# Kernel optimization log

Measured on AMD Instinct MI355X. Metric: run time of the kernel, lower is better.

The kernel has to match this reference:

```python
import jax, jax.numpy as jnp
import numpy as np

B, NAG = 8192, 16          # scenes, agents per scene
CIN, CH = 64, 128          # gnn_in_channels, gnn_out_channels
R2 = 8.0 * 8.0             # comm_range squared
BOX = 20.0                 # positions sampled uniformly in [0, BOX]^2


def _lin(k, fi, fo):
    k1, k2 = jax.random.split(k)
    s = 1.0 / np.sqrt(fi)
    W = jax.random.uniform(k1, (fi, fo), jnp.float32, -s, s)
    b = jax.random.uniform(k2, (fo,), jnp.float32, -s, s)
    return W, b


def setup_inputs() -> dict:
    key = jax.random.key(0)
    ks = jax.random.split(key, 10)
    x = jax.random.normal(ks[0], (B * NAG, CIN), jnp.float32)          # VAE mu per agent
    pos = jax.random.uniform(ks[1], (B, NAG, 2), jnp.float32) * BOX    # sensor xy positions
    W_rel1, b_rel1 = _lin(ks[2], CIN, CH)
    W_root1, _ = _lin(ks[3], CIN, CH)
    W_rel2, b_rel2 = _lin(ks[4], CH, CH)
    W_root2, _ = _lin(ks[5], CH, CH)
    Wh1, bh1 = _lin(ks[6], 2 * CH, 64)
    Wh2, bh2 = _lin(ks[7], 64, 32)
    Wh3, bh3 = _lin(ks[8], 32, 16)
    return dict(x=x, pos=pos, W_rel1=W_rel1, b_rel1=b_rel1, W_root1=W_root1,
                W_rel2=W_rel2, b_rel2=b_rel2, W_root2=W_root2,
                Wh1=Wh1, bh1=bh1, Wh2=Wh2, bh2=bh2, Wh3=Wh3, bh3=bh3)


def _graph_conv(h, adj, W_rel, b_rel, W_root):
    # PyG GraphConv (aggr='add'): out_i = W_rel @ sum_{j in N(i)} h_j + b_rel + W_root @ h_i
    nb = adj.shape[0]
    hb = h.reshape(nb, NAG, h.shape[-1])                 # [B, n, C]
    agg = jnp.einsum('bij,bjc->bic', adj, hb)            # neighbor sum within each scene
    return agg.reshape(h.shape[0], -1) @ W_rel + b_rel + h @ W_root


def reference(x, pos, W_rel1, b_rel1, W_root1, W_rel2, b_rel2, W_root2,
              Wh1, bh1, Wh2, bh2, Wh3, bh3):
    # radius_graph (batch-isolated, loop=False) as a per-scene dense mask
    diff = pos[:, :, None, :] - pos[:, None, :, :]       # [B, n, n, 2]
    d2 = jnp.sum(diff * diff, axis=-1)                   # [B, n, n]
    eye = jnp.eye(NAG, dtype=bool)
    adj = ((d2 <= R2) & ~eye).astype(x.dtype)            # [B, n, n]
    # Dropout(p=0.2) omitted (eval / deterministic reference).
    x1 = jax.nn.relu(_graph_conv(x, adj, W_rel1, b_rel1, W_root1))   # named 'x1' (inplace ReLU)
    x2 = jax.nn.relu(_graph_conv(x1, adj, W_rel2, b_rel2, W_root2))  # named 'x2' (inplace ReLU)
    h = jnp.concatenate([x1, x2], axis=-1)               # JumpingKnowledge('cat')
    h = jax.nn.relu(h @ Wh1 + bh1)
    h = jax.nn.relu(h @ Wh2 + bh2)
    out = h @ Wh3 + bh3                                  # [N, 16]
    return out.reshape(B, NAG, 16)
```

## Files before the change

kernel.cpp:

```cpp
#include <hip/hip_runtime.h>

#define NAG 16
#define SPB 4
#define NBLK 2048
#define R2f 64.0f

typedef unsigned short u16;
typedef __attribute__((ext_vector_type(8))) short short8;
typedef __attribute__((ext_vector_type(4))) float f32x4;

#define MFMA(a, b, c) __builtin_amdgcn_mfma_f32_16x16x32_bf16(a, b, c, 0, 0, 0)

#define OFF_B1 0
#define OFF_B2 16384
#define OFF_H1 49152
#define OFF_H2 65536
#define OFF_H3 67584
#define SWZ_UNITS 8512

__device__ __forceinline__ u16 f2b(float f) {
    unsigned u = __float_as_uint(f);
    unsigned r = u + 0x7FFFu + ((u >> 16) & 1u);
    return (u16)(r >> 16);
}
__device__ __forceinline__ unsigned rb(float f) {
    return (__float_as_uint(f) + 0x8000u) >> 16;
}
__device__ __forceinline__ unsigned pk2(float a, float b) {
    return ((__float_as_uint(a) + 0x8000u) >> 16) |
           ((__float_as_uint(b) + 0x8000u) & 0xFFFF0000u);
}

__global__ __launch_bounds__(256) void swizzle_w(
    const float* __restrict__ Wrel1, const float* __restrict__ Wroot1,
    const float* __restrict__ Wrel2, const float* __restrict__ Wroot2,
    const float* __restrict__ Wh1,  const float* __restrict__ Wh2,
    const float* __restrict__ Wh3,  u16* __restrict__ ws)
{
    const int u = blockIdx.x * 256 + threadIdx.x;
    if (u >= SWZ_UNITS) return;
    int v, T, N, ksplit;
    const float *W, *W2;
    u16* dst;
    if (u < 2048)      { v = u;        T = 8; N = 128; ksplit = 64;  W = Wroot1; W2 = Wrel1; dst = ws + OFF_B1 + v * 8; }
    else if (u < 6144) { v = u - 2048; T = 8; N = 128; ksplit = 128; W = Wroot2; W2 = Wrel2; dst = ws + OFF_B2 + v * 8; }
    else if (u < 8192) { v = u - 6144; T = 4; N = 64;  ksplit = 1 << 30; W = Wh1; W2 = Wh1; dst = ws + OFF_H1 + v * 8; }
    else if (u < 8448) { v = u - 8192; T = 2; N = 32;  ksplit = 1 << 30; W = Wh2; W2 = Wh2; dst = ws + OFF_H2 + v * 8; }
    else               { v = u - 8448; T = 1; N = 16;  ksplit = 1 << 30; W = Wh3; W2 = Wh3; dst = ws + OFF_H3 + v * 8; }
    const int lane = v & 63;
    const int t = (v >> 6) % T;
    const int s = (v >> 6) / T;
    const int n = t * 16 + (lane & 15);
    const int k0 = s * 32 + (lane >> 4) * 8;
    #pragma unroll
    for (int j = 0; j < 8; ++j) {
        const int k = k0 + j;
        const float val = (k < ksplit) ? W[k * N + n] : W2[(k - ksplit) * N + n];
        dst[j] = f2b(val);
    }
}

__device__ __forceinline__ short8 ldfrag(const u16* __restrict__ ws, int off,
                                         int T, int s, int tile, int lane) {
    return *(const short8*)(ws + off + (size_t)(((s * T + tile) * 64 + lane) * 8));
}

__device__ __forceinline__ short8 make_adjA(unsigned m, int q, int odd) {
    union { short8 v; unsigned u[4]; } r;
    const bool on = (q >> 1) == odd;
    const int base = (q & 1) * 8;
    #pragma unroll
    for (int jj = 0; jj < 4; ++jj) {
        const int k0 = base + 2 * jj;
        const unsigned lo = (on && ((m >> k0) & 1u)) ? 0x3F80u : 0u;
        const unsigned hi = (on && ((m >> (k0 + 1)) & 1u)) ? 0x3F80u : 0u;
        r.u[jj] = lo | (hi << 16);
    }
    return r.v;
}

__global__ __launch_bounds__(256) void gnn_fused5(
    const float* __restrict__ x, const float* __restrict__ pos,
    const float* __restrict__ brel1, const float* __restrict__ brel2,
    const float* __restrict__ bh1,  const float* __restrict__ bh2,
    const float* __restrict__ bh3,
    const u16* __restrict__ ws, float* __restrict__ out)
{
    __shared__ __align__(16) u16 pool[26624];
    __shared__ unsigned mask[64];
    u16* const xb  = pool;
    u16* const yT  = pool + 8704;
    u16* const x1b = pool + 17920;

    const int t = threadIdx.x;
    const int wv = t >> 6, lane = t & 63, ln = lane & 15, q = lane >> 4;
    const int c0 = 32 * wv;
    const int n0 = 2 * wv, n1 = 2 * wv + 1;
    const size_t sA = (size_t)blockIdx.x * SPB;

    {
        const int r = t >> 2, co = (t & 3) * 16;
        const float* src = x + (sA * 16 + r) * 64 + co;
        const float4 v0 = *(const float4*)(src);
        const float4 v1 = *(const float4*)(src + 4);
        const float4 v2 = *(const float4*)(src + 8);
        const float4 v3 = *(const float4*)(src + 12);
        uint4 ua, ub;
        ua.x = pk2(v0.x, v0.y); ua.y = pk2(v0.z, v0.w);
        ua.z = pk2(v1.x, v1.y); ua.w = pk2(v1.z, v1.w);
        ub.x = pk2(v2.x, v2.y); ub.y = pk2(v2.z, v2.w);
        ub.z = pk2(v3.x, v3.y); ub.w = pk2(v3.z, v3.w);
        *(uint4*)&xb[r * 136 + co]     = ua;
        *(uint4*)&xb[r * 136 + co + 8] = ub;
    }
    if (t < 64) {
        const int g = t >> 4, a = t & 15;
        const float* pp = pos + (sA + g) * (NAG * 2);
        const float ax = pp[2 * a], ay = pp[2 * a + 1];
        unsigned m = 0;
        for (int j = 0; j < NAG; ++j) {
            const float dx = ax - pp[2 * j], dy = ay - pp[2 * j + 1];
            if (dx * dx + dy * dy <= R2f && j != a) m |= (1u << j);
        }
        mask[g * 16 + a] = m;
    }
    __syncthreads();

    short8 adjA[4];
    #pragma unroll
    for (int g = 0; g < 4; ++g) adjA[g] = make_adjA(mask[g * 16 + ln], q, g & 1);

    {
        short8 Brl[2][2], Bro[2][2], Af[4][2];
        #pragma unroll
        for (int s = 0; s < 2; ++s) {
            Brl[s][0] = ldfrag(ws, OFF_B1, 8, s + 2, n0, lane);
            Brl[s][1] = ldfrag(ws, OFF_B1, 8, s + 2, n1, lane);
        }
        #pragma unroll
        for (int m = 0; m < 4; ++m) {
            Af[m][0] = *(const short8*)&xb[(m * 16 + ln) * 136 + q * 8];
            Af[m][1] = *(const short8*)&xb[(m * 16 + ln) * 136 + 32 + q * 8];
            f32x4 a0 = {0.f, 0.f, 0.f, 0.f}, a1 = a0;
            a0 = MFMA(Af[m][0], Brl[0][0], a0); a0 = MFMA(Af[m][1], Brl[1][0], a0);
            a1 = MFMA(Af[m][0], Brl[0][1], a1); a1 = MFMA(Af[m][1], Brl[1][1], a1);
            uint2 u0; u0.x = pk2(a0[0], a0[1]); u0.y = pk2(a0[2], a0[3]);
            uint2 u1; u1.x = pk2(a1[0], a1[1]); u1.y = pk2(a1[2], a1[3]);
            *(uint2*)&yT[(c0 + ln) * 72 + m * 16 + q * 4]      = u0;
            *(uint2*)&yT[(c0 + 16 + ln) * 72 + m * 16 + q * 4] = u1;
        }
        short8 By[2][2];
        #pragma unroll
        for (int w = 0; w < 2; ++w) {
            By[w][0] = *(const short8*)&yT[(c0 + ln) * 72 + w * 32 + q * 8];
            By[w][1] = *(const short8*)&yT[(c0 + 16 + ln) * 72 + w * 32 + q * 8];
        }
        #pragma unroll
        for (int s = 0; s < 2; ++s) {
            Bro[s][0] = ldfrag(ws, OFF_B1, 8, s, n0, lane);
            Bro[s][1] = ldfrag(ws, OFF_B1, 8, s, n1, lane);
        }
        const float b0 = brel1[c0 + ln], b1 = brel1[c0 + 16 + ln];
        #pragma unroll
        for (int g = 0; g < 4; ++g) {
            f32x4 a0 = {b0, b0, b0, b0}, a1 = {b1, b1, b1, b1};
            a0 = MFMA(Af[g][0], Bro[0][0], a0); a0 = MFMA(Af[g][1], Bro[1][0], a0);
            a1 = MFMA(Af[g][0], Bro[0][1], a1); a1 = MFMA(Af[g][1], Bro[1][1], a1);
            a0 = MFMA(adjA[g], By[g >> 1][0], a0);
            a1 = MFMA(adjA[g], By[g >> 1][1], a1);
            #pragma unroll
            for (int r = 0; r < 4; ++r) {
                const int row = g * 16 + q * 4 + r;
                x1b[row * 136 + c0 + ln]      = (u16)rb(fmaxf(a0[r], 0.f));
                x1b[row * 136 + c0 + 16 + ln] = (u16)rb(fmaxf(a1[r], 0.f));
            }
        }
    }
    __syncthreads();

    {
        short8 Brl[4][2];
        #pragma unroll
        for (int s = 0; s < 4; ++s) {
            Brl[s][0] = ldfrag(ws, OFF_B2, 8, s + 4, n0, lane);
            Brl[s][1] = ldfrag(ws, OFF_B2, 8, s + 4, n1, lane);
        }
        #pragma unroll
        for (int m = 0; m < 4; ++m) {
            f32x4 a0 = {0.f, 0.f, 0.f, 0.f}, a1 = a0;
            #pragma unroll
            for (int s = 0; s < 4; ++s) {
                const short8 A = *(const short8*)&x1b[(m * 16 + ln) * 136 + s * 32 + q * 8];
                a0 = MFMA(A, Brl[s][0], a0);
                a1 = MFMA(A, Brl[s][1], a1);
            }
            uint2 u0; u0.x = pk2(a0[0], a0[1]); u0.y = pk2(a0[2], a0[3]);
            uint2 u1; u1.x = pk2(a1[0], a1[1]); u1.y = pk2(a1[2], a1[3]);
            *(uint2*)&yT[(c0 + ln) * 72 + m * 16 + q * 4]      = u0;
            *(uint2*)&yT[(c0 + 16 + ln) * 72 + m * 16 + q * 4] = u1;
        }
        short8 By[2][2];
        #pragma unroll
        for (int w = 0; w < 2; ++w) {
            By[w][0] = *(const short8*)&yT[(c0 + ln) * 72 + w * 32 + q * 8];
            By[w][1] = *(const short8*)&yT[(c0 + 16 + ln) * 72 + w * 32 + q * 8];
        }
        short8 Bro[4][2];
        #pragma unroll
        for (int s = 0; s < 4; ++s) {
            Bro[s][0] = ldfrag(ws, OFF_B2, 8, s, n0, lane);
            Bro[s][1] = ldfrag(ws, OFF_B2, 8, s, n1, lane);
        }
        const float b0 = brel2[c0 + ln], b1 = brel2[c0 + 16 + ln];
        #pragma unroll
        for (int g = 0; g < 4; ++g) {
            f32x4 a0 = {b0, b0, b0, b0}, a1 = {b1, b1, b1, b1};
            #pragma unroll
            for (int s = 0; s < 4; ++s) {
                const short8 A = *(const short8*)&x1b[(g * 16 + ln) * 136 + s * 32 + q * 8];
                a0 = MFMA(A, Bro[s][0], a0);
                a1 = MFMA(A, Bro[s][1], a1);
            }
            a0 = MFMA(adjA[g], By[g >> 1][0], a0);
            a1 = MFMA(adjA[g], By[g >> 1][1], a1);
            #pragma unroll
            for (int r = 0; r < 4; ++r) {
                const int row = g * 16 + q * 4 + r;
                xb[row * 136 + c0 + ln]      = (u16)rb(fmaxf(a0[r], 0.f));
                xb[row * 136 + c0 + 16 + ln] = (u16)rb(fmaxf(a1[r], 0.f));
            }
        }
    }
    __syncthreads();

    {
        short8 Bf[8];
        #pragma unroll
        for (int s = 0; s < 8; ++s) Bf[s] = ldfrag(ws, OFF_H1, 4, s, wv, lane);
        const float b = bh1[wv * 16 + ln];
        #pragma unroll
        for (int m = 0; m < 4; ++m) {
            f32x4 a = {b, b, b, b}, c = {0.f, 0.f, 0.f, 0.f};
            #pragma unroll
            for (int s = 0; s < 4; ++s) {
                const short8 A1 = *(const short8*)&x1b[(m * 16 + ln) * 136 + s * 32 + q * 8];
                const short8 A2 = *(const short8*)&xb[(m * 16 + ln) * 136 + s * 32 + q * 8];
                a = MFMA(A1, Bf[s], a);
                c = MFMA(A2, Bf[s + 4], c);
            }
            #pragma unroll
            for (int r = 0; r < 4; ++r)
                yT[(m * 16 + q * 4 + r) * 72 + wv * 16 + ln] = (u16)rb(fmaxf(a[r] + c[r], 0.f));
        }
    }
    __syncthreads();

    {
        const u16* h1b = yT;
        u16* h2b = x1b;
        const short8 A0 = *(const short8*)&h1b[(wv * 16 + ln) * 72 + q * 8];
        const short8 A1 = *(const short8*)&h1b[(wv * 16 + ln) * 72 + 32 + q * 8];
        #pragma unroll
        for (int nt = 0; nt < 2; ++nt) {
            const short8 B0 = ldfrag(ws, OFF_H2, 2, 0, nt, lane);
            const short8 B1 = ldfrag(ws, OFF_H2, 2, 1, nt, lane);
            const float b = bh2[nt * 16 + ln];
            f32x4 a = {b, b, b, b};
            a = MFMA(A0, B0, a);
            a = MFMA(A1, B1, a);
            #pragma unroll
            for (int r = 0; r < 4; ++r)
                h2b[(wv * 16 + q * 4 + r) * 40 + nt * 16 + ln] = (u16)rb(fmaxf(a[r], 0.f));
        }
        const short8 A = *(const short8*)&h2b[(wv * 16 + ln) * 40 + q * 8];
        const short8 B = ldfrag(ws, OFF_H3, 1, 0, 0, lane);
        const float b = bh3[ln];
        f32x4 a = {b, b, b, b};
        a = MFMA(A, B, a);
        #pragma unroll
        for (int r = 0; r < 4; ++r)
            out[(sA * 16 + wv * 16 + q * 4 + r) * 16 + ln] = a[r];
    }
}

extern "C" void kernel_launch(void* const* d_in, const int* in_sizes, int n_in,
                              void* d_out, int out_size, void* d_ws, size_t ws_size,
                              hipStream_t stream) {
    const float* x      = (const float*)d_in[0];
    const float* pos    = (const float*)d_in[1];
    const float* Wrel1  = (const float*)d_in[2];
    const float* brel1  = (const float*)d_in[3];
    const float* Wroot1 = (const float*)d_in[4];
    const float* Wrel2  = (const float*)d_in[5];
    const float* brel2  = (const float*)d_in[6];
    const float* Wroot2 = (const float*)d_in[7];
    const float* Wh1    = (const float*)d_in[8];
    const float* bh1    = (const float*)d_in[9];
    const float* Wh2    = (const float*)d_in[10];
    const float* bh2    = (const float*)d_in[11];
    const float* Wh3    = (const float*)d_in[12];
    const float* bh3    = (const float*)d_in[13];
    u16* ws = (u16*)d_ws;

    swizzle_w<<<(SWZ_UNITS + 255) / 256, 256, 0, stream>>>(
        Wrel1, Wroot1, Wrel2, Wroot2, Wh1, Wh2, Wh3, ws);
    gnn_fused5<<<NBLK, 256, 0, stream>>>(
        x, pos, brel1, brel2, bh1, bh2, bh3, ws, (float*)d_out);
}
```

Before: 122.6 us.

## Halve scenes per block, compute adjacency masks in registers, reuse x1 fragments

Each block now handles two scenes instead of four, with twice as many blocks, and LDS usage is roughly halved to raise occupancy (launch bounds request 4 blocks/SM). Adjacency masks are computed redundantly per lane in registers rather than via a shared mask array and an extra sync. The layer-2 A fragments from x1 are kept in registers and reused for the root term and the head's first layer instead of re-read from LDS. In exchange, half the waves sit idle in the final head stage, weights are fetched twice as often overall, and the register pressure from held fragments may conflict with the occupancy target.

```diff
diff --git a/kernel.cpp b/kernel.cpp
--- a/kernel.cpp
+++ b/kernel.cpp
@@ -1,8 +1,8 @@
 #include <hip/hip_runtime.h>
 
 #define NAG 16
-#define SPB 4
-#define NBLK 2048
+#define SPB 2
+#define NBLK 4096
 #define R2f 64.0f
 
 typedef unsigned short u16;
@@ -79,18 +79,17 @@
     return r.v;
 }
 
-__global__ __launch_bounds__(256) void gnn_fused5(
+__global__ __launch_bounds__(256, 4) void gnn_fused5(
     const float* __restrict__ x, const float* __restrict__ pos,
     const float* __restrict__ brel1, const float* __restrict__ brel2,
     const float* __restrict__ bh1,  const float* __restrict__ bh2,
     const float* __restrict__ bh3,
     const u16* __restrict__ ws, float* __restrict__ out)
 {
-    __shared__ __align__(16) u16 pool[26624];
-    __shared__ unsigned mask[64];
+    __shared__ __align__(16) u16 pool[13824];
     u16* const xb  = pool;
-    u16* const yT  = pool + 8704;
-    u16* const x1b = pool + 17920;
+    u16* const yT  = pool + 4352;
+    u16* const x1b = pool + 9472;
 
     const int t = threadIdx.x;
     const int wv = t >> 6, lane = t & 63, ln = lane & 15, q = lane >> 4;
@@ -99,46 +98,42 @@
     const size_t sA = (size_t)blockIdx.x * SPB;
 
     {
-        const int r = t >> 2, co = (t & 3) * 16;
+        const int r = t >> 3, co = (t & 7) * 8;
         const float* src = x + (sA * 16 + r) * 64 + co;
         const float4 v0 = *(const float4*)(src);
         const float4 v1 = *(const float4*)(src + 4);
-        const float4 v2 = *(const float4*)(src + 8);
-        const float4 v3 = *(const float4*)(src + 12);
-        uint4 ua, ub;
+        uint4 ua;
         ua.x = pk2(v0.x, v0.y); ua.y = pk2(v0.z, v0.w);
         ua.z = pk2(v1.x, v1.y); ua.w = pk2(v1.z, v1.w);
-        ub.x = pk2(v2.x, v2.y); ub.y = pk2(v2.z, v2.w);
-        ub.z = pk2(v3.x, v3.y); ub.w = pk2(v3.z, v3.w);
-        *(uint4*)&xb[r * 136 + co]     = ua;
-        *(uint4*)&xb[r * 136 + co + 8] = ub;
-    }
-    if (t < 64) {
-        const int g = t >> 4, a = t & 15;
+        *(uint4*)&xb[r * 136 + co] = ua;
+    }
+    unsigned mk[2];
+    #pragma unroll
+    for (int g = 0; g < 2; ++g) {
         const float* pp = pos + (sA + g) * (NAG * 2);
-        const float ax = pp[2 * a], ay = pp[2 * a + 1];
+        const float ax = pp[2 * ln], ay = pp[2 * ln + 1];
         unsigned m = 0;
+        #pragma unroll
         for (int j = 0; j < NAG; ++j) {
             const float dx = ax - pp[2 * j], dy = ay - pp[2 * j + 1];
-            if (dx * dx + dy * dy <= R2f && j != a) m |= (1u << j);
-        }
-        mask[g * 16 + a] = m;
-    }
-    __syncthreads();
-
-    short8 adjA[4];
-    #pragma unroll
-    for (int g = 0; g < 4; ++g) adjA[g] = make_adjA(mask[g * 16 + ln], q, g & 1);
-
-    {
-        short8 Brl[2][2], Bro[2][2], Af[4][2];
+            if (dx * dx + dy * dy <= R2f && j != ln) m |= (1u << j);
+        }
+        mk[g] = m;
+    }
+    short8 adjA[2];
+    adjA[0] = make_adjA(mk[0], q, 0);
+    adjA[1] = make_adjA(mk[1], q, 1);
+    __syncthreads();
+
+    {
+        short8 Brl[2][2], Bro[2][2], Af[2][2];
         #pragma unroll
         for (int s = 0; s < 2; ++s) {
             Brl[s][0] = ldfrag(ws, OFF_B1, 8, s + 2, n0, lane);
             Brl[s][1] = ldfrag(ws, OFF_B1, 8, s + 2, n1, lane);
         }
         #pragma unroll
-        for (int m = 0; m < 4; ++m) {
+        for (int m = 0; m < 2; ++m) {
             Af[m][0] = *(const short8*)&xb[(m * 16 + ln) * 136 + q * 8];
             Af[m][1] = *(const short8*)&xb[(m * 16 + ln) * 136 + 32 + q * 8];
             f32x4 a0 = {0.f, 0.f, 0.f, 0.f}, a1 = a0;
@@ -146,15 +141,11 @@
             a1 = MFMA(Af[m][0], Brl[0][1], a1); a1 = MFMA(Af[m][1], Brl[1][1], a1);
             uint2 u0; u0.x = pk2(a0[0], a0[1]); u0.y = pk2(a0[2], a0[3]);
             uint2 u1; u1.x = pk2(a1[0], a1[1]); u1.y = pk2(a1[2], a1[3]);
-            *(uint2*)&yT[(c0 + ln) * 72 + m * 16 + q * 4]      = u0;
-            *(uint2*)&yT[(c0 + 16 + ln) * 72 + m * 16 + q * 4] = u1;
-        }
-        short8 By[2][2];
-        #pragma unroll
-        for (int w = 0; w < 2; ++w) {
-            By[w][0] = *(const short8*)&yT[(c0 + ln) * 72 + w * 32 + q * 8];
-            By[w][1] = *(const short8*)&yT[(c0 + 16 + ln) * 72 + w * 32 + q * 8];
-        }
+            *(uint2*)&yT[(c0 + ln) * 40 + m * 16 + q * 4]      = u0;
+            *(uint2*)&yT[(c0 + 16 + ln) * 40 + m * 16 + q * 4] = u1;
+        }
+        const short8 By0 = *(const short8*)&yT[(c0 + ln) * 40 + q * 8];
+        const short8 By1 = *(const short8*)&yT[(c0 + 16 + ln) * 40 + q * 8];
         #pragma unroll
         for (int s = 0; s < 2; ++s) {
             Bro[s][0] = ldfrag(ws, OFF_B1, 8, s, n0, lane);
@@ -162,12 +153,12 @@
         }
         const float b0 = brel1[c0 + ln], b1 = brel1[c0 + 16 + ln];
         #pragma unroll
-        for (int g = 0; g < 4; ++g) {
+        for (int g = 0; g < 2; ++g) {
             f32x4 a0 = {b0, b0, b0, b0}, a1 = {b1, b1, b1, b1};
             a0 = MFMA(Af[g][0], Bro[0][0], a0); a0 = MFMA(Af[g][1], Bro[1][0], a0);
             a1 = MFMA(Af[g][0], Bro[0][1], a1); a1 = MFMA(Af[g][1], Bro[1][1], a1);
-            a0 = MFMA(adjA[g], By[g >> 1][0], a0);
-            a1 = MFMA(adjA[g], By[g >> 1][1], a1);
+            a0 = MFMA(adjA[g], By0, a0);
+            a1 = MFMA(adjA[g], By1, a1);
             #pragma unroll
             for (int r = 0; r < 4; ++r) {
                 const int row = g * 16 + q * 4 + r;
@@ -178,33 +169,32 @@
     }
     __syncthreads();
 
-    {
-        short8 Brl[4][2];
-        #pragma unroll
-        for (int s = 0; s < 4; ++s) {
-            Brl[s][0] = ldfrag(ws, OFF_B2, 8, s + 4, n0, lane);
-            Brl[s][1] = ldfrag(ws, OFF_B2, 8, s + 4, n1, lane);
-        }
-        #pragma unroll
-        for (int m = 0; m < 4; ++m) {
-            f32x4 a0 = {0.f, 0.f, 0.f, 0.f}, a1 = a0;
+    short8 Af2[2][4];
+    {
+        {
+            short8 Brl[4][2];
             #pragma unroll
             for (int s = 0; s < 4; ++s) {
-                const short8 A = *(const short8*)&x1b[(m * 16 + ln) * 136 + s * 32 + q * 8];
-                a0 = MFMA(A, Brl[s][0], a0);
-                a1 = MFMA(A, Brl[s][1], a1);
-            }
-            uint2 u0; u0.x = pk2(a0[0], a0[1]); u0.y = pk2(a0[2], a0[3]);
-            uint2 u1; u1.x = pk2(a1[0], a1[1]); u1.y = pk2(a1[2], a1[3]);
-            *(uint2*)&yT[(c0 + ln) * 72 + m * 16 + q * 4]      = u0;
-            *(uint2*)&yT[(c0 + 16 + ln) * 72 + m * 16 + q * 4] = u1;
-        }
-        short8 By[2][2];
-        #pragma unroll
-        for (int w = 0; w < 2; ++w) {
-            By[w][0] = *(const short8*)&yT[(c0 + ln) * 72 + w * 32 + q * 8];
-            By[w][1] = *(const short8*)&yT[(c0 + 16 + ln) * 72 + w * 32 + q * 8];
-        }
+                Brl[s][0] = ldfrag(ws, OFF_B2, 8, s + 4, n0, lane);
+                Brl[s][1] = ldfrag(ws, OFF_B2, 8, s + 4, n1, lane);
+            }
+            #pragma unroll
+            for (int m = 0; m < 2; ++m) {
+                f32x4 a0 = {0.f, 0.f, 0.f, 0.f}, a1 = a0;
+                #pragma unroll
+                for (int s = 0; s < 4; ++s) {
+                    Af2[m][s] = *(const short8*)&x1b[(m * 16 + ln) * 136 + s * 32 + q * 8];
+                    a0 = MFMA(Af2[m][s], Brl[s][0], a0);
+                    a1 = MFMA(Af2[m][s], Brl[s][1], a1);
+                }
+                uint2 u0; u0.x = pk2(a0[0], a0[1]); u0.y = pk2(a0[2], a0[3]);
+                uint2 u1; u1.x = pk2(a1[0], a1[1]); u1.y = pk2(a1[2], a1[3]);
+                *(uint2*)&yT[(c0 + ln) * 40 + m * 16 + q * 4]      = u0;
+                *(uint2*)&yT[(c0 + 16 + ln) * 40 + m * 16 + q * 4] = u1;
+            }
+        }
+        const short8 By0 = *(const short8*)&yT[(c0 + ln) * 40 + q * 8];
+        const short8 By1 = *(const short8*)&yT[(c0 + 16 + ln) * 40 + q * 8];
         short8 Bro[4][2];
         #pragma unroll
         for (int s = 0; s < 4; ++s) {
@@ -213,16 +203,15 @@
         }
         const float b0 = brel2[c0 + ln], b1 = brel2[c0 + 16 + ln];
         #pragma unroll
-        for (int g = 0; g < 4; ++g) {
+        for (int g = 0; g < 2; ++g) {
             f32x4 a0 = {b0, b0, b0, b0}, a1 = {b1, b1, b1, b1};
             #pragma unroll
             for (int s = 0; s < 4; ++s) {
-                const short8 A = *(const short8*)&x1b[(g * 16 + ln) * 136 + s * 32 + q * 8];
-                a0 = MFMA(A, Bro[s][0], a0);
-                a1 = MFMA(A, Bro[s][1], a1);
-            }
-            a0 = MFMA(adjA[g], By[g >> 1][0], a0);
-            a1 = MFMA(adjA[g], By[g >> 1][1], a1);
+                a0 = MFMA(Af2[g][s], Bro[s][0], a0);
+                a1 = MFMA(Af2[g][s], Bro[s][1], a1);
+            }
+            a0 = MFMA(adjA[g], By0, a0);
+            a1 = MFMA(adjA[g], By1, a1);
             #pragma unroll
             for (int r = 0; r < 4; ++r) {
                 const int row = g * 16 + q * 4 + r;
@@ -239,13 +228,12 @@
         for (int s = 0; s < 8; ++s) Bf[s] = ldfrag(ws, OFF_H1, 4, s, wv, lane);
         const float b = bh1[wv * 16 + ln];
         #pragma unroll
-        for (int m = 0; m < 4; ++m) {
+        for (int m = 0; m < 2; ++m) {
             f32x4 a = {b, b, b, b}, c = {0.f, 0.f, 0.f, 0.f};
             #pragma unroll
             for (int s = 0; s < 4; ++s) {
-                const short8 A1 = *(const short8*)&x1b[(m * 16 + ln) * 136 + s * 32 + q * 8];
                 const short8 A2 = *(const short8*)&xb[(m * 16 + ln) * 136 + s * 32 + q * 8];
-                a = MFMA(A1, Bf[s], a);
+                a = MFMA(Af2[m][s], Bf[s], a);
                 c = MFMA(A2, Bf[s + 4], c);
             }
             #pragma unroll
@@ -255,7 +243,7 @@
     }
     __syncthreads();
 
-    {
+    if (wv < 2) {
         const u16* h1b = yT;
         u16* h2b = x1b;
         const short8 A0 = *(const short8*)&h1b[(wv * 16 + ln) * 72 + q * 8];
```

Measured after the change: 125.1 us. 2.0% more time.
